# Kernel optimization log

Measured on AMD Instinct MI355X. Metric: run time of the kernel, lower is better.

Reference implementation:

```python
import jax, jax.numpy as jnp
import numpy as np

D_MODEL = 1024
H = 16
DK = D_MODEL // H


def setup_inputs() -> dict:
    key = jax.random.key(0)
    ks = jax.random.split(key, 13)
    B, S = 2, 2048
    scale = 1.0 / np.sqrt(D_MODEL)
    inp = {
        "query": jax.random.normal(ks[0], (B, S, D_MODEL), jnp.float32),
        "key": jax.random.normal(ks[1], (B, S, D_MODEL), jnp.float32),
        "value": jax.random.normal(ks[2], (B, S, D_MODEL), jnp.float32),
        "mask": jax.random.randint(ks[3], (B, 1, S, S), 0, 2, jnp.int32),
        "Wq": jax.random.normal(ks[4], (D_MODEL, D_MODEL), jnp.float32) * scale,
        "bq": jnp.zeros((D_MODEL,), jnp.float32),
        "Wk": jax.random.normal(ks[5], (D_MODEL, D_MODEL), jnp.float32) * scale,
        "bk": jnp.zeros((D_MODEL,), jnp.float32),
        "Wv": jax.random.normal(ks[6], (D_MODEL, D_MODEL), jnp.float32) * scale,
        "bv": jnp.zeros((D_MODEL,), jnp.float32),
        "Wo": jax.random.normal(ks[7], (D_MODEL, D_MODEL), jnp.float32) * scale,
        "bo": jnp.zeros((D_MODEL,), jnp.float32),
    }
    return inp


def _split_heads(x, W, b):
    # torch Linear: x @ W.T + b; then [B,S,D] -> [B,H,S,DK]
    B, S, _ = x.shape
    out = x @ W.T + b
    return out.reshape(B, S, H, DK).transpose(0, 2, 1, 3)


def reference(query, key, value, mask, Wq, bq, Wk, bk, Wv, bv, Wo, bo):
    B, S, _ = query.shape
    q = _split_heads(query, Wq, bq)   # [B,H,S,DK]
    k = _split_heads(key, Wk, bk)
    v = _split_heads(value, Wv, bv)
    scores = jnp.einsum("bhqd,bhkd->bhqk", q, k) / jnp.sqrt(jnp.asarray(DK, q.dtype))
    scores = jnp.where(mask == 0, jnp.asarray(-1e9, scores.dtype), scores)
    prob = jax.nn.softmax(scores, axis=-1)
    out = jnp.einsum("bhqk,bhkd->bhqd", prob, v)  # [B,H,S,DK]
    out = out.transpose(0, 2, 1, 3).reshape(B, S, D_MODEL)
    return out @ Wo.T + bo
```

## Files before the change

### kernel.cpp

```cpp
#include <hip/hip_runtime.h>
#include <hip/hip_bf16.h>

#define B_   2
#define S_   2048
#define DM   1024
#define NH   16
#define Mdim 4096
#define Kdim 1024

typedef __attribute__((ext_vector_type(8))) short bf16x8;
typedef __attribute__((ext_vector_type(4))) float f32x4;

__device__ __forceinline__ short f2b(float x) {
  union { __hip_bfloat16 h; short s; } u;
  u.h = __float2bfloat16(x);
  return u.s;
}

__device__ __forceinline__ size_t blk_idx(int row, int k) {
  return ((size_t)(row >> 7) * 32 + (k >> 5)) * 4096 + (row & 127) * 32 + (k & 31);
}

__device__ __forceinline__ void async_copy16(const void* g, void* l) {
  __builtin_amdgcn_global_load_lds(
      (const __attribute__((address_space(1))) unsigned int*)g,
      (__attribute__((address_space(3))) unsigned int*)l, 16, 0, 0);
}

struct Cvt7 {
  const float* src[7];
  ushort* dst[7];
  int n[7];
};

__global__ __launch_bounds__(256) void cvt_all(Cvt7 c) {
  const int ten = blockIdx.y;
  const int tau = blockIdx.x;
  if (tau >= (c.n[ten] >> 12)) return;
  const int t = threadIdx.x;
  const int row = (tau >> 5) * 128 + (t >> 1);
  const int k = (tau & 31) * 32 + (t & 1) * 16;
  const float* s = c.src[ten] + (size_t)row * 1024 + k;
  ushort* d = c.dst[ten] + (size_t)tau * 4096 + t * 16;
#pragma unroll
  for (int h = 0; h < 2; ++h) {
    float4 a = *(const float4*)(s + h * 8);
    float4 b = *(const float4*)(s + h * 8 + 4);
    bf16x8 r;
    r[0] = f2b(a.x); r[1] = f2b(a.y); r[2] = f2b(a.z); r[3] = f2b(a.w);
    r[4] = f2b(b.x); r[5] = f2b(b.y); r[6] = f2b(b.z); r[7] = f2b(b.w);
    *(bf16x8*)(d + h * 8) = r;
  }
}

__global__ __launch_bounds__(256) void pack_mask(const int* __restrict__ mask,
                                                 unsigned long long* __restrict__ mpk) {
  const int gw = (blockIdx.x * 256 + threadIdx.x) >> 6;
  const int lane = threadIdx.x & 63;
  const int mv = mask[(size_t)gw * 64 + lane];
  const unsigned long long bits = __ballot(mv != 0);
  if (lane == 0) mpk[gw] = bits;
}

__global__ __launch_bounds__(256) void fill_bias(float* __restrict__ out,
                                                 const float* __restrict__ bias) {
  const int t = blockIdx.x * 256 + threadIdx.x;
  ((float4*)out)[t] = *(const float4*)&bias[(t * 4) & (DM - 1)];
}

struct Proj {
  const ushort* A[3];
  const ushort* W[3];
  const float* bias[3];
  ushort* out[3];
};

#define STAGE(buf, kb)                                  \
  do {                                                  \
    const size_t off = (size_t)(kb) * 4096;             \
    async_copy16(Ab + off, &a_s[buf][lo0]);             \
    async_copy16(Ab + off + 2048, &a_s[buf][lo1]);      \
    async_copy16(Wb + off, &b_s[buf][lo0]);             \
    async_copy16(Wb + off + 2048, &b_s[buf][lo1]);      \
  } while (0)

__global__ __launch_bounds__(256) void gemm_qkv(Proj p) {
  const int z = blockIdx.z;
  const int t = threadIdx.x;
  const int w = t >> 6, lane = t & 63;
  const int quad = lane >> 4, r16 = lane & 15;
  const int wr = w >> 1, wc = w & 1;
  const int row0 = blockIdx.x * 128, col0 = blockIdx.y * 128;

  __shared__ alignas(16) ushort a_s[2][4096];
  __shared__ alignas(16) ushort b_s[2][4096];

  const ushort* Ab = p.A[z] + (size_t)blockIdx.x * 32 * 4096 + (size_t)t * 8;
  const ushort* Wb = p.W[z] + (size_t)blockIdx.y * 32 * 4096 + (size_t)t * 8;
  const int lo0 = w * 512, lo1 = 2048 + w * 512;

  f32x4 acc[4][4];
#pragma unroll
  for (int mt = 0; mt < 4; ++mt)
#pragma unroll
    for (int nt = 0; nt < 4; ++nt) acc[mt][nt] = (f32x4){0.f, 0.f, 0.f, 0.f};

  STAGE(0, 0);
  int cur = 0;
  for (int kb = 0; kb < 32; ++kb) {
    __syncthreads();
    if (kb + 1 < 32) STAGE(1 - cur, kb + 1);
    bf16x8 af[4], bfr[4];
#pragma unroll
    for (int mt = 0; mt < 4; ++mt)
      af[mt] = *(const bf16x8*)&a_s[cur][(wr * 64 + mt * 16 + r16) * 32 + quad * 8];
#pragma unroll
    for (int nt = 0; nt < 4; ++nt)
      bfr[nt] = *(const bf16x8*)&b_s[cur][(wc * 64 + nt * 16 + r16) * 32 + quad * 8];
#pragma unroll
    for (int mt = 0; mt < 4; ++mt)
#pragma unroll
      for (int nt = 0; nt < 4; ++nt)
        acc[mt][nt] = __builtin_amdgcn_mfma_f32_16x16x32_bf16(af[mt], bfr[nt],
                                                              acc[mt][nt], 0, 0, 0);
    cur ^= 1;
  }

  const float scale = (z == 0) ? 0.125f : 1.0f;
  ushort* Cv = p.out[z];
#pragma unroll
  for (int mt = 0; mt < 4; ++mt) {
#pragma unroll
    for (int nt = 0; nt < 4; ++nt) {
      const int col = col0 + wc * 64 + nt * 16 + r16;
      const float bv = p.bias[z][col];
      const int rowb = row0 + wr * 64 + mt * 16 + quad * 4;
#pragma unroll
      for (int i = 0; i < 4; ++i) {
        const float v = (acc[mt][nt][i] + bv) * scale;
        const int row = rowb + i;
        const int bb = row >> 11, s = row & (S_ - 1);
        const int hh = col >> 6, d = col & 63;
        if (z == 0) {
          Cv[(size_t)row * DM + col] = (ushort)f2b(v);
        } else if (z == 1) {
          const size_t idx = ((size_t)(bb * NH + hh) * S_ + s) * 64 +
                             (((d >> 3) ^ (s & 7)) * 8) + (d & 7);
          Cv[idx] = (ushort)f2b(v);
        } else {
          const int s6 = s & 63;
          const int K16 = s6 >> 4, q4 = (s6 >> 2) & 3, ii = s6 & 3;
          const int pos = (K16 >> 1) * 32 + q4 * 8 + (K16 & 1) * 4 + ii;
          const size_t idx = ((size_t)(bb * NH + hh) * 64 + d) * S_ + (s & ~63) +
                             (((pos >> 3) ^ (d & 7)) * 8) + (pos & 7);
          Cv[idx] = (ushort)f2b(v);
        }
      }
    }
  }
}

__global__ __launch_bounds__(256) void gemm_out(const ushort* __restrict__ A,
                                                const ushort* __restrict__ W,
                                                float* __restrict__ out) {
  const int kz = blockIdx.z;
  const int t = threadIdx.x;
  const int w = t >> 6, lane = t & 63;
  const int quad = lane >> 4, r16 = lane & 15;
  const int wr = w >> 1, wc = w & 1;
  const int row0 = blockIdx.x * 128, col0 = blockIdx.y * 128;

  __shared__ alignas(16) ushort a_s[2][4096];
  __shared__ alignas(16) ushort b_s[2][4096];

  const ushort* Ab = A + (size_t)blockIdx.x * 32 * 4096 + (size_t)t * 8;
  const ushort* Wb = W + (size_t)blockIdx.y * 32 * 4096 + (size_t)t * 8;
  const int lo0 = w * 512, lo1 = 2048 + w * 512;

  f32x4 acc[4][4];
#pragma unroll
  for (int mt = 0; mt < 4; ++mt)
#pragma unroll
    for (int nt = 0; nt < 4; ++nt) acc[mt][nt] = (f32x4){0.f, 0.f, 0.f, 0.f};

  const int kb0 = kz * 16;
  STAGE(0, kb0);
  int cur = 0;
  for (int kb = kb0; kb < kb0 + 16; ++kb) {
    __syncthreads();
    if (kb + 1 < kb0 + 16) STAGE(1 - cur, kb + 1);
    bf16x8 af[4], bfr[4];
#pragma unroll
    for (int mt = 0; mt < 4; ++mt)
      af[mt] = *(const bf16x8*)&a_s[cur][(wr * 64 + mt * 16 + r16) * 32 + quad * 8];
#pragma unroll
    for (int nt = 0; nt < 4; ++nt)
      bfr[nt] = *(const bf16x8*)&b_s[cur][(wc * 64 + nt * 16 + r16) * 32 + quad * 8];
#pragma unroll
    for (int mt = 0; mt < 4; ++mt)
#pragma unroll
      for (int nt = 0; nt < 4; ++nt)
        acc[mt][nt] = __builtin_amdgcn_mfma_f32_16x16x32_bf16(af[mt], bfr[nt],
                                                              acc[mt][nt], 0, 0, 0);
    cur ^= 1;
  }
#undef STAGE

#pragma unroll
  for (int mt = 0; mt < 4; ++mt) {
#pragma unroll
    for (int nt = 0; nt < 4; ++nt) {
      const int col = col0 + wc * 64 + nt * 16 + r16;
      const int rowb = row0 + wr * 64 + mt * 16 + quad * 4;
#pragma unroll
      for (int i = 0; i < 4; ++i)
        unsafeAtomicAdd(&out[(size_t)(rowb + i) * DM + col], acc[mt][nt][i]);
    }
  }
}

__global__ __launch_bounds__(256) void attn_mfma(const ushort* __restrict__ Qp,
                                                 const ushort* __restrict__ Kg,
                                                 const ushort* __restrict__ Vg,
                                                 const unsigned long long* __restrict__ mpk,
                                                 ushort* __restrict__ Oa) {
  const int bh = blockIdx.y;
  const int b = bh >> 4, h = bh & 15;
  const int q0 = blockIdx.x * 64;
  const int t = threadIdx.x;
  const int w = t >> 6, lane = t & 63, quad = lane >> 4, r16 = lane & 15;
  const size_t rb = (size_t)b * S_;

  __shared__ alignas(16) ushort k_s[64 * 64];
  __shared__ alignas(16) ushort vt_s[64 * 64];

  const ushort* qptr = Qp + (rb + q0 + w * 16 + r16) * DM + h * 64 + quad * 8;
  const bf16x8 bq0 = *(const bf16x8*)qptr;
  const bf16x8 bq1 = *(const bf16x8*)(qptr + 32);

  float l_lane = 0.f;
  f32x4 oacc[4];
#pragma unroll
  for (int nt = 0; nt < 4; ++nt) oacc[nt] = (f32x4){0.f, 0.f, 0.f, 0.f};

  const ushort* kgb = Kg + (size_t)bh * S_ * 64 + (size_t)t * 8;
  const ushort* vgb = Vg + (size_t)bh * 64 * S_ + (size_t)(t >> 3) * S_ + (t & 7) * 8;
  ushort* kl0 = &k_s[w * 512];
  ushort* kl1 = &k_s[2048 + w * 512];
  ushort* vl0 = &vt_s[w * 512];
  ushort* vl1 = &vt_s[2048 + w * 512];

  const unsigned long long* mrowp = mpk + (rb + q0 + w * 16 + r16) * 32;

  for (int kt = 0; kt < S_; kt += 64) {
    __syncthreads();
    async_copy16(kgb + (size_t)kt * 64, kl0);
    async_copy16(kgb + (size_t)(kt + 32) * 64, kl1);
    async_copy16(vgb + kt, vl0);
    async_copy16(vgb + (size_t)32 * S_ + kt, vl1);
    __syncthreads();

    f32x4 sacc[4];
#pragma unroll
    for (int mt = 0; mt < 4; ++mt) {
      const int krow = mt * 16 + r16;
      const bf16x8 a0 = *(const bf16x8*)&k_s[krow * 64 + ((quad ^ (krow & 7)) * 8)];
      const bf16x8 a1 = *(const bf16x8*)&k_s[krow * 64 + (((4 + quad) ^ (krow & 7)) * 8)];
      f32x4 z = (f32x4){0.f, 0.f, 0.f, 0.f};
      z = __builtin_amdgcn_mfma_f32_16x16x32_bf16(a0, bq0, z, 0, 0, 0);
      sacc[mt] = __builtin_amdgcn_mfma_f32_16x16x32_bf16(a1, bq1, z, 0, 0, 0);
    }

    const unsigned long long mbits = mrowp[kt >> 6];
    bf16x8 pa0, pa1;
#pragma unroll
    for (int mt = 0; mt < 4; ++mt) {
#pragma unroll
      for (int i = 0; i < 4; ++i) {
        const unsigned int bit =
            (unsigned int)(mbits >> (mt * 16 + quad * 4 + i)) & 1u;
        const float p = bit ? __expf(sacc[mt][i]) : 0.f;
        l_lane += p;
        const short pb = f2b(p);
        if (mt < 2) pa0[(mt & 1) * 4 + i] = pb;
        else        pa1[(mt & 1) * 4 + i] = pb;
      }
    }

#pragma unroll
    for (int ks = 0; ks < 2; ++ks) {
      const bf16x8 pa = ks ? pa1 : pa0;
#pragma unroll
      for (int nt = 0; nt < 4; ++nt) {
        const int dk = nt * 16 + r16;
        const bf16x8 vb =
            *(const bf16x8*)&vt_s[dk * 64 + (((ks * 4 + quad) ^ (dk & 7)) * 8)];
        oacc[nt] = __builtin_amdgcn_mfma_f32_16x16x32_bf16(pa, vb, oacc[nt], 0, 0, 0);
      }
    }
  }

  l_lane += __shfl_xor(l_lane, 16);
  l_lane += __shfl_xor(l_lane, 32);
#pragma unroll
  for (int i = 0; i < 4; ++i) {
    const float lq = __shfl(l_lane, quad * 4 + i);
    const int row = (int)rb + q0 + w * 16 + quad * 4 + i;
#pragma unroll
    for (int nt = 0; nt < 4; ++nt) {
      const int col = h * 64 + nt * 16 + r16;
      Oa[blk_idx(row, col)] = (ushort)f2b(oacc[nt][i] / lq);
    }
  }
}

extern "C" void kernel_launch(void* const* d_in, const int* in_sizes, int n_in,
                              void* d_out, int out_size, void* d_ws, size_t ws_size,
                              hipStream_t stream) {
  const int* mask = (const int*)d_in[3];
  const float* bo = (const float*)d_in[11];

  const size_t NE = (size_t)B_ * S_ * DM;
  const size_t NW = (size_t)DM * DM;

  ushort* qc = (ushort*)d_ws;
  ushort* kc = qc + NE;
  ushort* vc = kc + NE;
  ushort* Qp = vc + NE;
  ushort* Kg = Qp + NE;
  ushort* Vg = Kg + NE;
  ushort* Wqc = Vg + NE;
  ushort* Wkc = Wqc + NW;
  ushort* Wvc = Wkc + NW;
  ushort* Woc = Wvc + NW;
  unsigned long long* mpk = (unsigned long long*)kc;

  Cvt7 c;
  const int sidx[7] = {0, 1, 2, 4, 6, 8, 10};
  ushort* dsts[7] = {qc, kc, vc, Wqc, Wkc, Wvc, Woc};
  for (int i = 0; i < 7; ++i) {
    c.src[i] = (const float*)d_in[sidx[i]];
    c.dst[i] = dsts[i];
    c.n[i] = (i < 3) ? (int)NE : (int)NW;
  }
  cvt_all<<<dim3(1024, 7), 256, 0, stream>>>(c);

  Proj p;
  p.A[0] = qc;  p.A[1] = kc;  p.A[2] = vc;
  p.W[0] = Wqc; p.W[1] = Wkc; p.W[2] = Wvc;
  p.bias[0] = (const float*)d_in[5];
  p.bias[1] = (const float*)d_in[7];
  p.bias[2] = (const float*)d_in[9];
  p.out[0] = Qp; p.out[1] = Kg; p.out[2] = Vg;
  gemm_qkv<<<dim3(Mdim / 128, DM / 128, 3), 256, 0, stream>>>(p);

  pack_mask<<<(B_ * S_ * (S_ / 64) * 64) / 256, 256, 0, stream>>>(mask, mpk);

  attn_mfma<<<dim3(S_ / 64, B_ * NH), 256, 0, stream>>>(Qp, Kg, Vg, mpk, qc);

  fill_bias<<<(int)(NE / 4 / 256), 256, 0, stream>>>((float*)d_out, bo);
  gemm_out<<<dim3(Mdim / 128, DM / 128, 2), 256, 0, stream>>>(qc, Woc, (float*)d_out);
}
```

Measured before the change: 307.4 us.

## Double-buffer attention K/V, stage QKV epilogue through LDS, fuse bias fill into prep

The attention loop now double-buffers K and V tiles in LDS, prefetching the next tile while computing on the current one and dropping one barrier per iteration. The QKV GEMM epilogue writes results into LDS in the target layout first, then stores coalesced 16-byte vectors instead of scattered 2-byte stores. The bias fill is folded into the conversion kernel as an extra grid row, removing one launch. pack_mask is rewritten to use vectorized int4 loads producing 16-bit words instead of a wave ballot. Together these aim to cut memory latency stalls and uncoalesced writes, at the cost of doubled attention LDS use and an extra barrier in the GEMM epilogue.

```diff
diff --git a/kernel.cpp b/kernel.cpp
--- a/kernel.cpp
+++ b/kernel.cpp
@@ -6,7 +6,6 @@
 #define DM   1024
 #define NH   16
 #define Mdim 4096
-#define Kdim 1024
 
 typedef __attribute__((ext_vector_type(8))) short bf16x8;
 typedef __attribute__((ext_vector_type(4))) float f32x4;
@@ -27,46 +26,63 @@
       (__attribute__((address_space(3))) unsigned int*)l, 16, 0, 0);
 }
 
-struct Cvt7 {
+struct Prep {
   const float* src[7];
   ushort* dst[7];
   int n[7];
+  float* out;
+  const float* bo;
 };
 
-__global__ __launch_bounds__(256) void cvt_all(Cvt7 c) {
-  const int ten = blockIdx.y;
-  const int tau = blockIdx.x;
-  if (tau >= (c.n[ten] >> 12)) return;
-  const int t = threadIdx.x;
-  const int row = (tau >> 5) * 128 + (t >> 1);
-  const int k = (tau & 31) * 32 + (t & 1) * 16;
-  const float* s = c.src[ten] + (size_t)row * 1024 + k;
-  ushort* d = c.dst[ten] + (size_t)tau * 4096 + t * 16;
-#pragma unroll
-  for (int h = 0; h < 2; ++h) {
-    float4 a = *(const float4*)(s + h * 8);
-    float4 b = *(const float4*)(s + h * 8 + 4);
-    bf16x8 r;
-    r[0] = f2b(a.x); r[1] = f2b(a.y); r[2] = f2b(a.z); r[3] = f2b(a.w);
-    r[4] = f2b(b.x); r[5] = f2b(b.y); r[6] = f2b(b.z); r[7] = f2b(b.w);
-    *(bf16x8*)(d + h * 8) = r;
+__global__ __launch_bounds__(256) void prep(Prep p) {
+  const int y = blockIdx.y, x = blockIdx.x, t = threadIdx.x;
+  if (y < 7) {
+    if (x >= (p.n[y] >> 12)) return;
+    const int row = (x >> 5) * 128 + (t >> 1);
+    const int k = (x & 31) * 32 + (t & 1) * 16;
+    const float* s = p.src[y] + (size_t)row * 1024 + k;
+    ushort* d = p.dst[y] + (size_t)x * 4096 + t * 16;
+#pragma unroll
+    for (int h = 0; h < 2; ++h) {
+      float4 a = *(const float4*)(s + h * 8);
+      float4 b = *(const float4*)(s + h * 8 + 4);
+      bf16x8 r;
+      r[0] = f2b(a.x); r[1] = f2b(a.y); r[2] = f2b(a.z); r[3] = f2b(a.w);
+      r[4] = f2b(b.x); r[5] = f2b(b.y); r[6] = f2b(b.z); r[7] = f2b(b.w);
+      *(bf16x8*)(d + h * 8) = r;
+    }
+  } else {
+    const size_t t8 = ((size_t)x * 256 + t) * 8;
+    const int col = (int)(t8 & (DM - 1));
+    *(float4*)(p.out + t8) = *(const float4*)&p.bo[col];
+    *(float4*)(p.out + t8 + 4) = *(const float4*)&p.bo[col + 4];
   }
 }
 
 __global__ __launch_bounds__(256) void pack_mask(const int* __restrict__ mask,
-                                                 unsigned long long* __restrict__ mpk) {
-  const int gw = (blockIdx.x * 256 + threadIdx.x) >> 6;
-  const int lane = threadIdx.x & 63;
-  const int mv = mask[(size_t)gw * 64 + lane];
-  const unsigned long long bits = __ballot(mv != 0);
-  if (lane == 0) mpk[gw] = bits;
-}
-
-__global__ __launch_bounds__(256) void fill_bias(float* __restrict__ out,
-                                                 const float* __restrict__ bias) {
-  const int t = blockIdx.x * 256 + threadIdx.x;
-  ((float4*)out)[t] = *(const float4*)&bias[(t * 4) & (DM - 1)];
-}
+                                                 ushort* __restrict__ mpk16) {
+  const int g = blockIdx.x * 256 + threadIdx.x;
+  const int4* m4 = (const int4*)(mask + (size_t)g * 16);
+  unsigned int bits = 0;
+#pragma unroll
+  for (int q = 0; q < 4; ++q) {
+    const int4 m = m4[q];
+    bits |= (m.x != 0 ? 1u : 0u) << (q * 4 + 0);
+    bits |= (m.y != 0 ? 1u : 0u) << (q * 4 + 1);
+    bits |= (m.z != 0 ? 1u : 0u) << (q * 4 + 2);
+    bits |= (m.w != 0 ? 1u : 0u) << (q * 4 + 3);
+  }
+  mpk16[g] = (ushort)bits;
+}
+
+#define STAGE(buf, kb)                                        \
+  do {                                                        \
+    const size_t off = (size_t)(kb) * 4096;                   \
+    async_copy16(Ab + off, &smem[buf][lo0]);                  \
+    async_copy16(Ab + off + 2048, &smem[buf][lo1]);           \
+    async_copy16(Wb + off, &smem[buf][4096 + lo0]);           \
+    async_copy16(Wb + off + 2048, &smem[buf][4096 + lo1]);    \
+  } while (0)
 
 struct Proj {
   const ushort* A[3];
@@ -74,15 +90,6 @@
   const float* bias[3];
   ushort* out[3];
 };
-
-#define STAGE(buf, kb)                                  \
-  do {                                                  \
-    const size_t off = (size_t)(kb) * 4096;             \
-    async_copy16(Ab + off, &a_s[buf][lo0]);             \
-    async_copy16(Ab + off + 2048, &a_s[buf][lo1]);      \
-    async_copy16(Wb + off, &b_s[buf][lo0]);             \
-    async_copy16(Wb + off + 2048, &b_s[buf][lo1]);      \
-  } while (0)
 
 __global__ __launch_bounds__(256) void gemm_qkv(Proj p) {
   const int z = blockIdx.z;
@@ -92,8 +99,7 @@
   const int wr = w >> 1, wc = w & 1;
   const int row0 = blockIdx.x * 128, col0 = blockIdx.y * 128;
 
-  __shared__ alignas(16) ushort a_s[2][4096];
-  __shared__ alignas(16) ushort b_s[2][4096];
+  __shared__ alignas(16) ushort smem[2][8192];
 
   const ushort* Ab = p.A[z] + (size_t)blockIdx.x * 32 * 4096 + (size_t)t * 8;
   const ushort* Wb = p.W[z] + (size_t)blockIdx.y * 32 * 4096 + (size_t)t * 8;
@@ -113,10 +119,10 @@
     bf16x8 af[4], bfr[4];
 #pragma unroll
     for (int mt = 0; mt < 4; ++mt)
-      af[mt] = *(const bf16x8*)&a_s[cur][(wr * 64 + mt * 16 + r16) * 32 + quad * 8];
+      af[mt] = *(const bf16x8*)&smem[cur][(wr * 64 + mt * 16 + r16) * 32 + quad * 8];
 #pragma unroll
     for (int nt = 0; nt < 4; ++nt)
-      bfr[nt] = *(const bf16x8*)&b_s[cur][(wc * 64 + nt * 16 + r16) * 32 + quad * 8];
+      bfr[nt] = *(const bf16x8*)&smem[cur][4096 + (wc * 64 + nt * 16 + r16) * 32 + quad * 8];
 #pragma unroll
     for (int mt = 0; mt < 4; ++mt)
 #pragma unroll
@@ -126,39 +132,67 @@
     cur ^= 1;
   }
 
+  ushort* c_s = &smem[0][0];
   const float scale = (z == 0) ? 0.125f : 1.0f;
-  ushort* Cv = p.out[z];
+  __syncthreads();
 #pragma unroll
   for (int mt = 0; mt < 4; ++mt) {
 #pragma unroll
     for (int nt = 0; nt < 4; ++nt) {
-      const int col = col0 + wc * 64 + nt * 16 + r16;
-      const float bv = p.bias[z][col];
-      const int rowb = row0 + wr * 64 + mt * 16 + quad * 4;
+      const int c = wc * 64 + nt * 16 + r16;
+      const float bv = p.bias[z][col0 + c];
 #pragma unroll
       for (int i = 0; i < 4; ++i) {
+        const int row = wr * 64 + mt * 16 + quad * 4 + i;
         const float v = (acc[mt][nt][i] + bv) * scale;
-        const int row = rowb + i;
-        const int bb = row >> 11, s = row & (S_ - 1);
-        const int hh = col >> 6, d = col & 63;
+        int off;
         if (z == 0) {
-          Cv[(size_t)row * DM + col] = (ushort)f2b(v);
+          off = row * 128 + c;
         } else if (z == 1) {
-          const size_t idx = ((size_t)(bb * NH + hh) * S_ + s) * 64 +
-                             (((d >> 3) ^ (s & 7)) * 8) + (d & 7);
-          Cv[idx] = (ushort)f2b(v);
+          const int d = c & 63, hh = c >> 6;
+          off = hh * 8192 + row * 64 + (((d >> 3) ^ (row & 7)) * 8) + (d & 7);
         } else {
-          const int s6 = s & 63;
-          const int K16 = s6 >> 4, q4 = (s6 >> 2) & 3, ii = s6 & 3;
-          const int pos = (K16 >> 1) * 32 + q4 * 8 + (K16 & 1) * 4 + ii;
-          const size_t idx = ((size_t)(bb * NH + hh) * 64 + d) * S_ + (s & ~63) +
-                             (((pos >> 3) ^ (d & 7)) * 8) + (pos & 7);
-          Cv[idx] = (ushort)f2b(v);
+          const int s6 = row & 63;
+          const int pos = ((s6 >> 5) & 1) * 32 + ((s6 >> 2) & 3) * 8 +
+                          ((s6 >> 4) & 1) * 4 + (s6 & 3);
+          const int d = c & 63, hh = c >> 6, sb = row >> 6;
+          off = (hh * 2 + sb) * 4096 + d * 64 + (((pos >> 3) ^ (d & 7)) * 8) + (pos & 7);
         }
+        c_s[off] = (ushort)f2b(v);
       }
     }
   }
-}
+  __syncthreads();
+
+  const int bb = row0 >> 11;
+  const int s0 = row0 & (S_ - 1);
+  const int h0 = col0 >> 6;
+  if (z == 0) {
+    ushort* dst = p.out[0] + (size_t)row0 * DM + col0;
+#pragma unroll
+    for (int it = 0; it < 8; ++it) {
+      const int lin = it * 256 + t, row = lin >> 4, ch = lin & 15;
+      *(bf16x8*)(dst + (size_t)row * DM + ch * 8) = *(const bf16x8*)&c_s[row * 128 + ch * 8];
+    }
+  } else if (z == 1) {
+#pragma unroll
+    for (int it = 0; it < 8; ++it) {
+      const int lin = it * 256 + t, hh = lin >> 10, wi = lin & 1023;
+      ushort* dst = p.out[1] + ((size_t)(bb * NH + h0 + hh) * S_ + s0) * 64;
+      *(bf16x8*)(dst + wi * 8) = *(const bf16x8*)&c_s[hh * 8192 + wi * 8];
+    }
+  } else {
+#pragma unroll
+    for (int it = 0; it < 8; ++it) {
+      const int lin = it * 256 + t, reg = lin >> 9, wi = lin & 511;
+      const int hh = reg >> 1, sb = reg & 1, d = wi >> 3, ko = (wi & 7) * 8;
+      ushort* dst = p.out[2] + ((size_t)(bb * NH + h0 + hh) * 64 + d) * S_ +
+                    s0 + sb * 64 + ko;
+      *(bf16x8*)dst = *(const bf16x8*)&c_s[reg * 4096 + wi * 8];
+    }
+  }
+}
+
 
 __global__ __launch_bounds__(256) void gemm_out(const ushort* __restrict__ A,
                                                 const ushort* __restrict__ W,
@@ -170,8 +204,7 @@
   const int wr = w >> 1, wc = w & 1;
   const int row0 = blockIdx.x * 128, col0 = blockIdx.y * 128;
 
-  __shared__ alignas(16) ushort a_s[2][4096];
-  __shared__ alignas(16) ushort b_s[2][4096];
+  __shared__ alignas(16) ushort smem[2][8192];
 
   const ushort* Ab = A + (size_t)blockIdx.x * 32 * 4096 + (size_t)t * 8;
   const ushort* Wb = W + (size_t)blockIdx.y * 32 * 4096 + (size_t)t * 8;
@@ -192,10 +225,10 @@
     bf16x8 af[4], bfr[4];
 #pragma unroll
     for (int mt = 0; mt < 4; ++mt)
-      af[mt] = *(const bf16x8*)&a_s[cur][(wr * 64 + mt * 16 + r16) * 32 + quad * 8];
+      af[mt] = *(const bf16x8*)&smem[cur][(wr * 64 + mt * 16 + r16) * 32 + quad * 8];
 #pragma unroll
     for (int nt = 0; nt < 4; ++nt)
-      bfr[nt] = *(const bf16x8*)&b_s[cur][(wc * 64 + nt * 16 + r16) * 32 + quad * 8];
+      bfr[nt] = *(const bf16x8*)&smem[cur][4096 + (wc * 64 + nt * 16 + r16) * 32 + quad * 8];
 #pragma unroll
     for (int mt = 0; mt < 4; ++mt)
 #pragma unroll
@@ -231,8 +264,8 @@
   const int w = t >> 6, lane = t & 63, quad = lane >> 4, r16 = lane & 15;
   const size_t rb = (size_t)b * S_;
 
-  __shared__ alignas(16) ushort k_s[64 * 64];
-  __shared__ alignas(16) ushort vt_s[64 * 64];
+  __shared__ alignas(16) ushort k_s[2][4096];
+  __shared__ alignas(16) ushort vt_s[2][4096];
 
   const ushort* qptr = Qp + (rb + q0 + w * 16 + r16) * DM + h * 64 + quad * 8;
   const bf16x8 bq0 = *(const bf16x8*)qptr;
@@ -245,30 +278,32 @@
 
   const ushort* kgb = Kg + (size_t)bh * S_ * 64 + (size_t)t * 8;
   const ushort* vgb = Vg + (size_t)bh * 64 * S_ + (size_t)(t >> 3) * S_ + (t & 7) * 8;
-  ushort* kl0 = &k_s[w * 512];
-  ushort* kl1 = &k_s[2048 + w * 512];
-  ushort* vl0 = &vt_s[w * 512];
-  ushort* vl1 = &vt_s[2048 + w * 512];
+
+#define ASTAGE(buf, kt)                                                   \
+  do {                                                                    \
+    async_copy16(kgb + (size_t)(kt) * 64, &k_s[buf][w * 512]);            \
+    async_copy16(kgb + (size_t)((kt) + 32) * 64, &k_s[buf][2048 + w * 512]); \
+    async_copy16(vgb + (kt), &vt_s[buf][w * 512]);                        \
+    async_copy16(vgb + (size_t)32 * S_ + (kt), &vt_s[buf][2048 + w * 512]); \
+  } while (0)
 
   const unsigned long long* mrowp = mpk + (rb + q0 + w * 16 + r16) * 32;
 
+  ASTAGE(0, 0);
+  int cur = 0;
   for (int kt = 0; kt < S_; kt += 64) {
     __syncthreads();
-    async_copy16(kgb + (size_t)kt * 64, kl0);
-    async_copy16(kgb + (size_t)(kt + 32) * 64, kl1);
-    async_copy16(vgb + kt, vl0);
-    async_copy16(vgb + (size_t)32 * S_ + kt, vl1);
-    __syncthreads();
+    if (kt + 64 < S_) ASTAGE(cur ^ 1, kt + 64);
 
     f32x4 sacc[4];
 #pragma unroll
     for (int mt = 0; mt < 4; ++mt) {
       const int krow = mt * 16 + r16;
-      const bf16x8 a0 = *(const bf16x8*)&k_s[krow * 64 + ((quad ^ (krow & 7)) * 8)];
-      const bf16x8 a1 = *(const bf16x8*)&k_s[krow * 64 + (((4 + quad) ^ (krow & 7)) * 8)];
-      f32x4 z = (f32x4){0.f, 0.f, 0.f, 0.f};
-      z = __builtin_amdgcn_mfma_f32_16x16x32_bf16(a0, bq0, z, 0, 0, 0);
-      sacc[mt] = __builtin_amdgcn_mfma_f32_16x16x32_bf16(a1, bq1, z, 0, 0, 0);
+      const bf16x8 a0 = *(const bf16x8*)&k_s[cur][krow * 64 + ((quad ^ (krow & 7)) * 8)];
+      const bf16x8 a1 = *(const bf16x8*)&k_s[cur][krow * 64 + (((4 + quad) ^ (krow & 7)) * 8)];
+      f32x4 zz = (f32x4){0.f, 0.f, 0.f, 0.f};
+      zz = __builtin_amdgcn_mfma_f32_16x16x32_bf16(a0, bq0, zz, 0, 0, 0);
+      sacc[mt] = __builtin_amdgcn_mfma_f32_16x16x32_bf16(a1, bq1, zz, 0, 0, 0);
     }
 
     const unsigned long long mbits = mrowp[kt >> 6];
@@ -294,11 +329,13 @@
       for (int nt = 0; nt < 4; ++nt) {
         const int dk = nt * 16 + r16;
         const bf16x8 vb =
-            *(const bf16x8*)&vt_s[dk * 64 + (((ks * 4 + quad) ^ (dk & 7)) * 8)];
+            *(const bf16x8*)&vt_s[cur][dk * 64 + (((ks * 4 + quad) ^ (dk & 7)) * 8)];
         oacc[nt] = __builtin_amdgcn_mfma_f32_16x16x32_bf16(pa, vb, oacc[nt], 0, 0, 0);
       }
     }
-  }
+    cur ^= 1;
+  }
+#undef ASTAGE
 
   l_lane += __shfl_xor(l_lane, 16);
   l_lane += __shfl_xor(l_lane, 32);
@@ -318,7 +355,6 @@
                               void* d_out, int out_size, void* d_ws, size_t ws_size,
                               hipStream_t stream) {
   const int* mask = (const int*)d_in[3];
-  const float* bo = (const float*)d_in[11];
 
   const size_t NE = (size_t)B_ * S_ * DM;
   const size_t NW = (size_t)DM * DM;
@@ -335,15 +371,17 @@
   ushort* Woc = Wvc + NW;
   unsigned long long* mpk = (unsigned long long*)kc;
 
-  Cvt7 c;
+  Prep pr;
   const int sidx[7] = {0, 1, 2, 4, 6, 8, 10};
   ushort* dsts[7] = {qc, kc, vc, Wqc, Wkc, Wvc, Woc};
   for (int i = 0; i < 7; ++i) {
-    c.src[i] = (const float*)d_in[sidx[i]];
-    c.dst[i] = dsts[i];
-    c.n[i] = (i < 3) ? (int)NE : (int)NW;
-  }
-  cvt_all<<<dim3(1024, 7), 256, 0, stream>>>(c);
+    pr.src[i] = (const float*)d_in[sidx[i]];
+    pr.dst[i] = dsts[i];
+    pr.n[i] = (i < 3) ? (int)NE : (int)NW;
+  }
+  pr.out = (float*)d_out;
+  pr.bo = (const float*)d_in[11];
+  prep<<<dim3(2048, 8), 256, 0, stream>>>(pr);
 
   Proj p;
   p.A[0] = qc;  p.A[1] = kc;  p.A[2] = vc;
@@ -354,10 +392,9 @@
   p.out[0] = Qp; p.out[1] = Kg; p.out[2] = Vg;
   gemm_qkv<<<dim3(Mdim / 128, DM / 128, 3), 256, 0, stream>>>(p);
 
-  pack_mask<<<(B_ * S_ * (S_ / 64) * 64) / 256, 256, 0, stream>>>(mask, mpk);
+  pack_mask<<<2048, 256, 0, stream>>>(mask, (ushort*)mpk);
 
   attn_mfma<<<dim3(S_ / 64, B_ * NH), 256, 0, stream>>>(Qp, Kg, Vg, mpk, qc);
 
-  fill_bias<<<(int)(NE / 4 / 256), 256, 0, stream>>>((float*)d_out, bo);
   gemm_out<<<dim3(Mdim / 128, DM / 128, 2), 256, 0, stream>>>(qc, Woc, (float*)d_out);
 }
```

Result: faster. 299.0 us (-2.7%).
